# Optimization experiments

Measured on AMD Instinct MI355X. Metric: run time of the kernel, lower is better.

Reference implementation:

```python
import jax, jax.numpy as jnp
import numpy as np

# irreps_in = irreps_out = 32x0e + 16x1o ; irreps_sh = 1x0e + 1x1o
MUL0, MUL1 = 32, 16
N_NODES = 12000
N_EDGES = 120000
INV_SQRT3 = float(1.0 / np.sqrt(3.0))   # w3j(1,1,0), w3j(0,1,1), w3j(1,0,1) coefficient
SQRT2 = float(np.sqrt(2.0))             # e3nn normalize2mom constant for ReLU
# e3nn TP norms: irrep_normalization='component', path_normalization='element'.
# Each output irrep receives paths with num_elements 32 and 16 -> x = 48.
N_0E = float(1.0 / np.sqrt(48.0))       # alpha = dim(0e)/48 = 1/48
N_1O = float(np.sqrt(3.0 / 48.0))       # alpha = dim(1o)/48 = 3/48
# uvw weight blocks (mul2 = 1): (s,y0->s),(s,y0->g),(v,y1->s),(v,y1->g),(s,y1->v),(v,y0->v)
SPLITS = [MUL0 * MUL0, MUL0 * MUL1, MUL1 * MUL0, MUL1 * MUL1, MUL0 * MUL1, MUL1 * MUL1]
OFFS = np.cumsum([0] + SPLITS)
WNUM = int(OFFS[-1])  # 3072


def setup_inputs() -> dict:
    key = jax.random.key(0)
    k1, k2, k3, k4, k5 = jax.random.split(key, 5)
    x = jax.random.normal(k1, (N_NODES, MUL0 + 3 * MUL1), dtype=jnp.float32)
    edge_attr = jax.random.normal(k2, (N_EDGES, 64), dtype=jnp.float32)
    Yij = jax.random.normal(k3, (N_EDGES, 4), dtype=jnp.float32)
    edge_index = jax.random.randint(k4, (2, N_EDGES), 0, N_NODES, dtype=jnp.int64)
    w_emb = jax.random.normal(k5, (2 * MUL0 + 64, WNUM), dtype=jnp.float32)
    return {"x": x, "edge_attr": edge_attr, "Yij": Yij,
            "edge_index": edge_index, "w_emb": w_emb}


def reference(x, edge_attr, Yij, edge_index, w_emb):
    dst, src = edge_index[0], edge_index[1]
    E = edge_attr.shape[0]
    xs = x[:, :MUL0]                                   # [N, 32] scalars (0e)
    xv = x[:, MUL0:].reshape(-1, MUL1, 3)              # [N, 16, 3] vectors (1o)

    # per-edge weight MLP (single e3nn FC layer, weight scaled by 1/sqrt(fan_in))
    emb = jnp.concatenate([xs[dst], xs[src], edge_attr], axis=-1)     # [E, 128]
    w = emb @ (w_emb / np.sqrt(w_emb.shape[0]))                       # [E, 3072]
    Ws = [w[:, OFFS[i]:OFFS[i + 1]] for i in range(6)]
    W1 = Ws[0].reshape(E, MUL0, MUL0)
    W2 = Ws[1].reshape(E, MUL0, MUL1)
    W3 = Ws[2].reshape(E, MUL1, MUL0)
    W4 = Ws[3].reshape(E, MUL1, MUL1)
    W5 = Ws[4].reshape(E, MUL0, MUL1)
    W6 = Ws[5].reshape(E, MUL1, MUL1)

    # gather source features, split sh
    x1s, x1v = xs[src], xv[src]                        # [E,32], [E,16,3]
    y0, y1 = Yij[:, 0], Yij[:, 1:4]                    # [E], [E,3]

    sy0 = x1s * y0[:, None]                            # 0e x 0e paths
    vdot = jnp.einsum('euk,ek->eu', x1v, y1) * INV_SQRT3  # 1o x 1o -> 0e
    out_s = N_0E * (jnp.einsum('euw,eu->ew', W1, sy0) +
                    jnp.einsum('euw,eu->ew', W3, vdot))    # [E, 32]
    out_g = N_0E * (jnp.einsum('euw,eu->ew', W2, sy0) +
                    jnp.einsum('euw,eu->ew', W4, vdot))    # [E, 16]
    out_v = (N_1O * INV_SQRT3) * (
        jnp.einsum('euw,eu,ek->ewk', W5, x1s, y1) +
        jnp.einsum('euw,euk->ewk', W6, x1v * y0[:, None, None]))  # [E, 16, 3]

    msg = jnp.concatenate([out_s, out_g, out_v.reshape(E, MUL1 * 3)], axis=-1)  # [E, 96]

    # scatter mean onto destination nodes
    summed = jax.ops.segment_sum(msg, dst, num_segments=N_NODES)
    cnt = jax.ops.segment_sum(jnp.ones((E,), msg.dtype), dst, num_segments=N_NODES)
    mean = summed / jnp.maximum(cnt, 1.0)[:, None]

    # Gate (e3nn Activation normalizes ReLU by sqrt(2))
    s = SQRT2 * jax.nn.relu(mean[:, :MUL0])
    g = SQRT2 * jax.nn.relu(mean[:, MUL0:MUL0 + MUL1])
    v = mean[:, MUL0 + MUL1:].reshape(-1, MUL1, 3) * g[:, :, None]
    out = jnp.concatenate([s, v.reshape(-1, MUL1 * 3)], axis=-1)     # [N, 80]
    return x + out
```

## Files before the change

### kernel.cpp

```cpp
#include <hip/hip_runtime.h>
#include <hip/hip_bf16.h>

#define E_EDGES 120000
#define NUM_NODES 12000

typedef __attribute__((ext_vector_type(8))) short bfrag;
typedef __attribute__((ext_vector_type(8))) unsigned short ushort8;
typedef __attribute__((ext_vector_type(4))) float f32x4;

#define INV_SQRT3 0.57735026918962576f
#define SQRT2_C   1.41421356237309515f
#define N_0E_C    0.14433756729740643f
#define NV_C      0.14433756729740643f
#define WSCALE    0.08838834764831845f

__device__ __forceinline__ unsigned short f2bf(float f) {
    union { float f; unsigned int u; } v; v.f = f;
    unsigned int r = v.u + 0x7fffu + ((v.u >> 16) & 1u);
    return (unsigned short)(r >> 16);
}

__device__ __forceinline__ ushort8 pack8(f32x4 a, f32x4 b) {
    ushort8 o;
    o[0] = f2bf(a.x); o[1] = f2bf(a.y); o[2] = f2bf(a.z); o[3] = f2bf(a.w);
    o[4] = f2bf(b.x); o[5] = f2bf(b.y); o[6] = f2bf(b.z); o[7] = f2bf(b.w);
    return o;
}

__global__ void k_wt(const float* __restrict__ w_emb, unsigned short* __restrict__ Bt) {
    int o = blockIdx.x * 256 + threadIdx.x;
    if (o >= 3072 * 128) return;
    int t = o >> 11;
    int c = (o >> 3) & 255;
    int j = o & 7;
    int kb = c >> 6;
    int quad = (c >> 4) & 3;
    int col = c & 15;
    int k = kb * 32 + quad * 8 + j;
    int n = t * 16 + col;
    Bt[o] = f2bf(w_emb[k * 3072 + n] * WSCALE);
}

__global__ void k_count(const int* __restrict__ edge_index, int* __restrict__ cnt) {
    int e = blockIdx.x * 256 + threadIdx.x;
    if (e >= E_EDGES) return;
    atomicAdd(cnt + edge_index[e], 1);
}

__global__ void k_scan(const int* __restrict__ cnt, int* __restrict__ offs) {
    __shared__ int psum[256];
    int t = threadIdx.x;
    const int SEG = (NUM_NODES + 255) / 256;
    int lo = t * SEG;
    int hi = lo + SEG; if (hi > NUM_NODES) hi = NUM_NODES;
    int s = 0;
    for (int i = lo; i < hi; ++i) s += cnt[i];
    psum[t] = s;
    __syncthreads();
    if (t == 0) {
        int acc = 0;
        for (int i = 0; i < 256; ++i) { int v = psum[i]; psum[i] = acc; acc += v; }
    }
    __syncthreads();
    int acc = psum[t];
    for (int i = lo; i < hi; ++i) { offs[i] = acc; acc += cnt[i]; }
    if (t == 255) offs[NUM_NODES] = acc;
}

__global__ void k_scatter(const int* __restrict__ edge_index, const int* __restrict__ offs,
                          int* __restrict__ cursor, int* __restrict__ perm_src) {
    int e = blockIdx.x * 256 + threadIdx.x;
    if (e >= E_EDGES) return;
    int d = edge_index[e];
    int p = offs[d] + atomicAdd(cursor + d, 1);
    perm_src[p] = e;
}

__global__ __launch_bounds__(320) void k_prep(
    const float* __restrict__ x, const float* __restrict__ edge_attr,
    const float* __restrict__ Yij, const int* __restrict__ edge_index,
    unsigned short* __restrict__ emb, float* __restrict__ rT) {
    const int wid = threadIdx.x >> 6;
    const int lane = threadIdx.x & 63;
    const long e = (long)blockIdx.x * 64 + lane;
    const int src = edge_index[E_EDGES + e];
    const float* xs = x + (long)src * 80;
    const f32x4 y = *(const f32x4*)(Yij + 4 * e);

    if (wid == 4) {
        const int dst = edge_index[e];
        const float* xd = x + (long)dst * 80;
        const float* ea = edge_attr + (long)e * 64;
        ushort8* embp = (ushort8*)(emb + (long)e * 128);
#pragma unroll
        for (int cb = 0; cb < 4; ++cb)
            embp[cb] = pack8(*(const f32x4*)(xd + cb * 8), *(const f32x4*)(xd + cb * 8 + 4));
#pragma unroll
        for (int cb = 0; cb < 4; ++cb)
            embp[4 + cb] = pack8(*(const f32x4*)(xs + cb * 8), *(const f32x4*)(xs + cb * 8 + 4));
#pragma unroll
        for (int cb = 0; cb < 8; ++cb)
            embp[8 + cb] = pack8(*(const f32x4*)(ea + cb * 8), *(const f32x4*)(ea + cb * 8 + 4));
    } else if (wid == 0) {
        const float y0 = y.x;
#pragma unroll
        for (int i = 0; i < 8; ++i) {
            f32x4 v = *(const f32x4*)(xs + i * 4);
            rT[(long)(4 * i + 0) * E_EDGES + e] = v.x * y0;
            rT[(long)(4 * i + 1) * E_EDGES + e] = v.y * y0;
            rT[(long)(4 * i + 2) * E_EDGES + e] = v.z * y0;
            rT[(long)(4 * i + 3) * E_EDGES + e] = v.w * y0;
        }
    } else if (wid == 1) {
        const float y1a = y.y, y1b = y.z, y1c = y.w;
        float xv[48];
#pragma unroll
        for (int i = 0; i < 12; ++i) {
            f32x4 v = *(const f32x4*)(xs + 32 + i * 4);
            xv[4 * i] = v.x; xv[4 * i + 1] = v.y; xv[4 * i + 2] = v.z; xv[4 * i + 3] = v.w;
        }
#pragma unroll
        for (int u = 0; u < 16; ++u)
            rT[(long)(32 + u) * E_EDGES + e] =
                (xv[3 * u] * y1a + xv[3 * u + 1] * y1b + xv[3 * u + 2] * y1c) * INV_SQRT3;
#pragma unroll
        for (int i = 0; i < 4; ++i) {
            f32x4 v = *(const f32x4*)(xs + i * 4);
            rT[(long)(48 + 4 * i + 0) * E_EDGES + e] = v.x;
            rT[(long)(48 + 4 * i + 1) * E_EDGES + e] = v.y;
            rT[(long)(48 + 4 * i + 2) * E_EDGES + e] = v.z;
            rT[(long)(48 + 4 * i + 3) * E_EDGES + e] = v.w;
        }
    } else if (wid == 2) {
        const float y0 = y.x;
#pragma unroll
        for (int i = 0; i < 4; ++i) {
            f32x4 v = *(const f32x4*)(xs + 16 + i * 4);
            rT[(long)(64 + 4 * i + 0) * E_EDGES + e] = v.x;
            rT[(long)(64 + 4 * i + 1) * E_EDGES + e] = v.y;
            rT[(long)(64 + 4 * i + 2) * E_EDGES + e] = v.z;
            rT[(long)(64 + 4 * i + 3) * E_EDGES + e] = v.w;
        }
#pragma unroll
        for (int i = 0; i < 4; ++i) {
            f32x4 v = *(const f32x4*)(xs + 32 + i * 4);
            rT[(long)(80 + 4 * i + 0) * E_EDGES + e] = v.x * y0;
            rT[(long)(80 + 4 * i + 1) * E_EDGES + e] = v.y * y0;
            rT[(long)(80 + 4 * i + 2) * E_EDGES + e] = v.z * y0;
            rT[(long)(80 + 4 * i + 3) * E_EDGES + e] = v.w * y0;
        }
    } else {
        const float y0 = y.x;
#pragma unroll
        for (int i = 0; i < 8; ++i) {
            f32x4 v = *(const f32x4*)(xs + 48 + i * 4);
            rT[(long)(96 + 4 * i + 0) * E_EDGES + e] = v.x * y0;
            rT[(long)(96 + 4 * i + 1) * E_EDGES + e] = v.y * y0;
            rT[(long)(96 + 4 * i + 2) * E_EDGES + e] = v.z * y0;
            rT[(long)(96 + 4 * i + 3) * E_EDGES + e] = v.w * y0;
        }
    }
}

__global__ __launch_bounds__(256, 4) void k_gemm(
    const unsigned short* __restrict__ emb, const unsigned short* __restrict__ Bt,
    const float* __restrict__ rT, const float* __restrict__ Yij,
    float* __restrict__ msg) {
    const int lane = threadIdx.x & 63;
    const int wave = threadIdx.x >> 6;
    long e0 = (long)blockIdx.x * 128 + (long)wave * 32;
    const bool dup = (e0 + 32 > E_EDGES);
    if (dup) e0 = E_EDGES - 32;
    const int col = lane & 15, quad = lane >> 4;

    __shared__ __align__(16) char lds[2][16384];

    bfrag A[2][4];
#pragma unroll
    for (int s = 0; s < 2; ++s) {
        const unsigned short* ap = emb + (e0 + s * 16 + col) * 128 + quad * 8;
#pragma unroll
        for (int kb = 0; kb < 4; ++kb) A[s][kb] = *(const bfrag*)(ap + kb * 32);
    }

    auto stage = [&](int ci) {
        const char* g = (const char*)Bt + (size_t)ci * 16384 + wave * 4096 + lane * 16;
        char* l = &lds[ci & 1][wave * 4096];
#pragma unroll
        for (int j = 0; j < 4; ++j)
            __builtin_amdgcn_global_load_lds(
                (const __attribute__((address_space(1))) unsigned int*)(g + j * 1024),
                (__attribute__((address_space(3))) unsigned int*)(l + j * 1024), 16, 0, 0);
    };

    f32x4 z = {0.f, 0.f, 0.f, 0.f};
    f32x4 acc_s0[2] = {z, z}, acc_s1[2] = {z, z}, acc_g[2] = {z, z}, acc_t5[2] = {z, z};
    f32x4 acc_v[2][3] = {{z, z, z}, {z, z, z}};

    const float* rbase = rT + e0 + quad * 4;
    auto loadw = [&](int r, f32x4& a, f32x4& b) {
        const float* p = rbase + (long)r * E_EDGES;
        a = *(const f32x4*)(p);
        b = *(const f32x4*)(p + 16);
    };

    auto tile = [&](const char* lt, f32x4& c0, f32x4& c1) {
        bfrag B0 = *(const bfrag*)(lt + lane * 16);
        bfrag B1 = *(const bfrag*)(lt + lane * 16 + 1024);
        bfrag B2 = *(const bfrag*)(lt + lane * 16 + 2048);
        bfrag B3 = *(const bfrag*)(lt + lane * 16 + 3072);
        c0 = z; c1 = z;
        c0 = __builtin_amdgcn_mfma_f32_16x16x32_bf16(A[0][0], B0, c0, 0, 0, 0);
        c1 = __builtin_amdgcn_mfma_f32_16x16x32_bf16(A[1][0], B0, c1, 0, 0, 0);
        c0 = __builtin_amdgcn_mfma_f32_16x16x32_bf16(A[0][1], B1, c0, 0, 0, 0);
        c1 = __builtin_amdgcn_mfma_f32_16x16x32_bf16(A[1][1], B1, c1, 0, 0, 0);
        c0 = __builtin_amdgcn_mfma_f32_16x16x32_bf16(A[0][2], B2, c0, 0, 0, 0);
        c1 = __builtin_amdgcn_mfma_f32_16x16x32_bf16(A[1][2], B2, c1, 0, 0, 0);
        c0 = __builtin_amdgcn_mfma_f32_16x16x32_bf16(A[0][3], B3, c0, 0, 0, 0);
        c1 = __builtin_amdgcn_mfma_f32_16x16x32_bf16(A[1][3], B3, c1, 0, 0, 0);
    };

    stage(0);
    int cidx = 0;
    auto nextbuf = [&]() -> const char* {
        __syncthreads();
        if (cidx + 1 < 48) stage(cidx + 1);
        const char* b = lds[cidx & 1];
        ++cidx;
        return b;
    };

    f32x4 c0, c1;

    {
        f32x4 p0a, p0b, p1a, p1b;
        loadw(0, p0a, p0b); loadw(1, p1a, p1b);
#pragma unroll 1
        for (int j = 0; j < 16; ++j) {
            const char* buf = nextbuf();
            f32x4 w0a = p0a, w0b = p0b, w1a = p1a, w1b = p1b;
            int nr = (j < 15) ? (2 * j + 2) : 0;
            loadw(nr, p0a, p0b); loadw(nr + 1, p1a, p1b);
            tile(buf,         c0, c1); acc_s0[0] += c0 * w0a; acc_s0[1] += c1 * w0b;
            tile(buf + 4096,  c0, c1); acc_s1[0] += c0 * w0a; acc_s1[1] += c1 * w0b;
            tile(buf + 8192,  c0, c1); acc_s0[0] += c0 * w1a; acc_s0[1] += c1 * w1b;
            tile(buf + 12288, c0, c1); acc_s1[0] += c0 * w1a; acc_s1[1] += c1 * w1b;
        }
    }
    {
        f32x4 pa[4], pb[4];
#pragma unroll
        for (int i = 0; i < 4; ++i) loadw(i, pa[i], pb[i]);
#pragma unroll 1
        for (int j = 0; j < 8; ++j) {
            const char* buf = nextbuf();
            f32x4 wa[4], wb[4];
#pragma unroll
            for (int i = 0; i < 4; ++i) { wa[i] = pa[i]; wb[i] = pb[i]; }
            int nr = (j < 7) ? (4 * j + 4) : 0;
#pragma unroll
            for (int i = 0; i < 4; ++i) loadw(nr + i, pa[i], pb[i]);
#pragma unroll
            for (int i = 0; i < 4; ++i) {
                tile(buf + i * 4096, c0, c1);
                acc_g[0] += c0 * wa[i]; acc_g[1] += c1 * wb[i];
            }
        }
    }
    {
        f32x4 p0a, p0b, p1a, p1b;
        loadw(32, p0a, p0b); loadw(33, p1a, p1b);
#pragma unroll 1
        for (int j = 0; j < 8; ++j) {
            const char* buf = nextbuf();
            f32x4 w0a = p0a, w0b = p0b, w1a = p1a, w1b = p1b;
            int nr = (j < 7) ? (32 + 2 * j + 2) : 32;
            loadw(nr, p0a, p0b); loadw(nr + 1, p1a, p1b);
            tile(buf,         c0, c1); acc_s0[0] += c0 * w0a; acc_s0[1] += c1 * w0b;
            tile(buf + 4096,  c0, c1); acc_s1[0] += c0 * w0a; acc_s1[1] += c1 * w0b;
            tile(buf + 8192,  c0, c1); acc_s0[0] += c0 * w1a; acc_s0[1] += c1 * w1b;
            tile(buf + 12288, c0, c1); acc_s1[0] += c0 * w1a; acc_s1[1] += c1 * w1b;
        }
    }
    {
        f32x4 pa[4], pb[4];
#pragma unroll
        for (int i = 0; i < 4; ++i) loadw(32 + i, pa[i], pb[i]);
#pragma unroll 1
        for (int j = 0; j < 4; ++j) {
            const char* buf = nextbuf();
            f32x4 wa[4], wb[4];
#pragma unroll
            for (int i = 0; i < 4; ++i) { wa[i] = pa[i]; wb[i] = pb[i]; }
            int nr = (j < 3) ? (32 + 4 * j + 4) : 32;
#pragma unroll
            for (int i = 0; i < 4; ++i) loadw(nr + i, pa[i], pb[i]);
#pragma unroll
            for (int i = 0; i < 4; ++i) {
                tile(buf + i * 4096, c0, c1);
                acc_g[0] += c0 * wa[i]; acc_g[1] += c1 * wb[i];
            }
        }
    }
    {
        f32x4 pa[4], pb[4];
#pragma unroll
        for (int i = 0; i < 4; ++i) loadw(48 + i, pa[i], pb[i]);
#pragma unroll 1
        for (int j = 0; j < 8; ++j) {
            const char* buf = nextbuf();
            f32x4 wa[4], wb[4];
#pragma unroll
            for (int i = 0; i < 4; ++i) { wa[i] = pa[i]; wb[i] = pb[i]; }
            int nr = (j < 7) ? (48 + 4 * j + 4) : 48;
#pragma unroll
            for (int i = 0; i < 4; ++i) loadw(nr + i, pa[i], pb[i]);
#pragma unroll
            for (int i = 0; i < 4; ++i) {
                tile(buf + i * 4096, c0, c1);
                acc_t5[0] += c0 * wa[i]; acc_t5[1] += c1 * wb[i];
            }
        }
    }
    {
        f32x4 va[3], vb[3];
#pragma unroll
        for (int k = 0; k < 3; ++k) loadw(80 + k, va[k], vb[k]);
#pragma unroll 1
        for (int j = 0; j < 4; ++j) {
            const char* buf = nextbuf();
#pragma unroll
            for (int i = 0; i < 4; ++i) {
                f32x4 wa[3], wb[3];
#pragma unroll
                for (int k = 0; k < 3; ++k) { wa[k] = va[k]; wb[k] = vb[k]; }
                int un = 4 * j + i + 1; if (un > 15) un = 0;
#pragma unroll
                for (int k = 0; k < 3; ++k) loadw(80 + 3 * un + k, va[k], vb[k]);
                tile(buf + i * 4096, c0, c1);
#pragma unroll
                for (int k = 0; k < 3; ++k) {
                    acc_v[0][k] += c0 * wa[k];
                    acc_v[1][k] += c1 * wb[k];
                }
            }
        }
    }

    if (dup) return;
#pragma unroll
    for (int s = 0; s < 2; ++s) {
        long eb = e0 + s * 16 + quad * 4;
#pragma unroll
        for (int r = 0; r < 4; ++r) {
            long e = eb + r;
            float* base = msg + e * 96;
            float y1a = Yij[4 * e + 1], y1b = Yij[4 * e + 2], y1c = Yij[4 * e + 3];
            base[col]            = N_0E_C * acc_s0[s][r];
            base[col + 16]       = N_0E_C * acc_s1[s][r];
            base[32 + col]       = N_0E_C * acc_g[s][r];
            float t5 = acc_t5[s][r];
            base[48 + col * 3 + 0] = NV_C * (t5 * y1a + acc_v[s][0][r]);
            base[48 + col * 3 + 1] = NV_C * (t5 * y1b + acc_v[s][1][r]);
            base[48 + col * 3 + 2] = NV_C * (t5 * y1c + acc_v[s][2][r]);
        }
    }
}

__global__ __launch_bounds__(128) void k_nodesum(
    const float* __restrict__ msg, const int* __restrict__ perm_src,
    const int* __restrict__ offs, const float* __restrict__ x,
    float* __restrict__ out) {
    int n = blockIdx.x;
    int t = threadIdx.x;
    int lo = offs[n], hi = offs[n + 1];
    float s = 0.0f;
    if (t < 96) {
        for (int i = lo; i < hi; ++i) {
            int p = perm_src[i];
            s += msg[(long)p * 96 + t];
        }
    }
    float inv = 1.0f / fmaxf((float)(hi - lo), 1.0f);
    __shared__ float sm[96];
    if (t < 96) sm[t] = s * inv;
    __syncthreads();
    if (t < 80) {
        float val;
        if (t < 32) {
            val = SQRT2_C * fmaxf(sm[t], 0.0f);
        } else {
            int j = t - 32;
            int w = j / 3;
            float g = SQRT2_C * fmaxf(sm[32 + w], 0.0f);
            val = sm[48 + j] * g;
        }
        out[(long)n * 80 + t] = x[(long)n * 80 + t] + val;
    }
}

extern "C" void kernel_launch(void* const* d_in, const int* in_sizes, int n_in,
                              void* d_out, int out_size, void* d_ws, size_t ws_size,
                              hipStream_t stream) {
    const float* x         = (const float*)d_in[0];
    const float* edge_attr = (const float*)d_in[1];
    const float* Yij       = (const float*)d_in[2];
    const int*   edge_index= (const int*)d_in[3];
    const float* w_emb     = (const float*)d_in[4];
    float* out = (float*)d_out;

    char* ws = (char*)d_ws;
    size_t off = 0;
    unsigned short* emb = (unsigned short*)(ws + off); off += (size_t)E_EDGES * 128 * 2;
    unsigned short* Bt  = (unsigned short*)(ws + off); off += (size_t)3072 * 128 * 2;
    off = (off + 255) & ~(size_t)255;
    float* rT      = (float*)(ws + off); off += (size_t)128 * E_EDGES * 4;
    float* msg     = (float*)(ws + off); off += (size_t)E_EDGES * 96 * 4;
    int*   perm_src= (int*)(ws + off);   off += (size_t)E_EDGES * 4;
    int*   offs    = (int*)(ws + off);   off += (size_t)(NUM_NODES + 1) * 4;
    size_t zoff = off;
    int*   cnt     = (int*)(ws + off);   off += (size_t)NUM_NODES * 4;
    int*   cursor  = (int*)(ws + off);   off += (size_t)NUM_NODES * 4;

    hipMemsetAsync(ws + zoff, 0, (size_t)NUM_NODES * 2 * 4, stream);
    k_wt     <<<(3072 * 128 + 255) / 256, 256, 0, stream>>>(w_emb, Bt);
    k_count  <<<(E_EDGES + 255) / 256, 256, 0, stream>>>(edge_index, cnt);
    k_scan   <<<1, 256, 0, stream>>>(cnt, offs);
    k_scatter<<<(E_EDGES + 255) / 256, 256, 0, stream>>>(edge_index, offs, cursor, perm_src);
    k_prep   <<<E_EDGES / 64, 320, 0, stream>>>(x, edge_attr, Yij, edge_index, emb, rT);
    k_gemm   <<<(E_EDGES + 127) / 128, 256, 0, stream>>>(emb, Bt, rT, Yij, msg);
    k_nodesum<<<NUM_NODES, 128, 0, stream>>>(msg, perm_src, offs, x, out);
}
```

Measured before the change: 320.3 us.

## Process edges in destination-sorted order and tile rT per 64-edge block

The prep kernel now reads edges through the destination-sorted permutation. Embeddings, per-edge factors and a copied Yij vector are therefore written in sorted order, so messages come out grouped by destination node. The node reduction can then sum a contiguous run of message rows instead of gathering them through perm_src. The rT buffer also moves from a full-length transposed layout to 64-edge tiles of 128 rows, which keeps the GEMM's per-row loads local. In exchange, edge_attr and Yij reads in prep become random gathers, and a 16-byte-per-edge ys buffer adds write and read traffic.

```diff
diff --git a/kernel.cpp b/kernel.cpp
--- a/kernel.cpp
+++ b/kernel.cpp
@@ -79,19 +79,23 @@
 __global__ __launch_bounds__(320) void k_prep(
     const float* __restrict__ x, const float* __restrict__ edge_attr,
     const float* __restrict__ Yij, const int* __restrict__ edge_index,
-    unsigned short* __restrict__ emb, float* __restrict__ rT) {
+    const int* __restrict__ perm_src,
+    unsigned short* __restrict__ emb, float* __restrict__ rT,
+    f32x4* __restrict__ ys) {
     const int wid = threadIdx.x >> 6;
     const int lane = threadIdx.x & 63;
-    const long e = (long)blockIdx.x * 64 + lane;
-    const int src = edge_index[E_EDGES + e];
+    const long p = (long)blockIdx.x * 64 + lane;
+    const int eid = perm_src[p];
+    const int src = edge_index[E_EDGES + eid];
     const float* xs = x + (long)src * 80;
-    const f32x4 y = *(const f32x4*)(Yij + 4 * e);
+    const f32x4 y = *(const f32x4*)(Yij + 4 * (long)eid);
+    float* tb = rT + (size_t)blockIdx.x * 8192 + lane;
 
     if (wid == 4) {
-        const int dst = edge_index[e];
+        const int dst = edge_index[eid];
         const float* xd = x + (long)dst * 80;
-        const float* ea = edge_attr + (long)e * 64;
-        ushort8* embp = (ushort8*)(emb + (long)e * 128);
+        const float* ea = edge_attr + (long)eid * 64;
+        ushort8* embp = (ushort8*)(emb + (long)p * 128);
 #pragma unroll
         for (int cb = 0; cb < 4; ++cb)
             embp[cb] = pack8(*(const f32x4*)(xd + cb * 8), *(const f32x4*)(xd + cb * 8 + 4));
@@ -106,11 +110,12 @@
 #pragma unroll
         for (int i = 0; i < 8; ++i) {
             f32x4 v = *(const f32x4*)(xs + i * 4);
-            rT[(long)(4 * i + 0) * E_EDGES + e] = v.x * y0;
-            rT[(long)(4 * i + 1) * E_EDGES + e] = v.y * y0;
-            rT[(long)(4 * i + 2) * E_EDGES + e] = v.z * y0;
-            rT[(long)(4 * i + 3) * E_EDGES + e] = v.w * y0;
-        }
+            tb[(4 * i + 0) * 64] = v.x * y0;
+            tb[(4 * i + 1) * 64] = v.y * y0;
+            tb[(4 * i + 2) * 64] = v.z * y0;
+            tb[(4 * i + 3) * 64] = v.w * y0;
+        }
+        ys[p] = y;
     } else if (wid == 1) {
         const float y1a = y.y, y1b = y.z, y1c = y.w;
         float xv[48];
@@ -121,50 +126,50 @@
         }
 #pragma unroll
         for (int u = 0; u < 16; ++u)
-            rT[(long)(32 + u) * E_EDGES + e] =
+            tb[(32 + u) * 64] =
                 (xv[3 * u] * y1a + xv[3 * u + 1] * y1b + xv[3 * u + 2] * y1c) * INV_SQRT3;
 #pragma unroll
         for (int i = 0; i < 4; ++i) {
             f32x4 v = *(const f32x4*)(xs + i * 4);
-            rT[(long)(48 + 4 * i + 0) * E_EDGES + e] = v.x;
-            rT[(long)(48 + 4 * i + 1) * E_EDGES + e] = v.y;
-            rT[(long)(48 + 4 * i + 2) * E_EDGES + e] = v.z;
-            rT[(long)(48 + 4 * i + 3) * E_EDGES + e] = v.w;
+            tb[(48 + 4 * i + 0) * 64] = v.x;
+            tb[(48 + 4 * i + 1) * 64] = v.y;
+            tb[(48 + 4 * i + 2) * 64] = v.z;
+            tb[(48 + 4 * i + 3) * 64] = v.w;
         }
     } else if (wid == 2) {
         const float y0 = y.x;
 #pragma unroll
         for (int i = 0; i < 4; ++i) {
             f32x4 v = *(const f32x4*)(xs + 16 + i * 4);
-            rT[(long)(64 + 4 * i + 0) * E_EDGES + e] = v.x;
-            rT[(long)(64 + 4 * i + 1) * E_EDGES + e] = v.y;
-            rT[(long)(64 + 4 * i + 2) * E_EDGES + e] = v.z;
-            rT[(long)(64 + 4 * i + 3) * E_EDGES + e] = v.w;
+            tb[(64 + 4 * i + 0) * 64] = v.x;
+            tb[(64 + 4 * i + 1) * 64] = v.y;
+            tb[(64 + 4 * i + 2) * 64] = v.z;
+            tb[(64 + 4 * i + 3) * 64] = v.w;
         }
 #pragma unroll
         for (int i = 0; i < 4; ++i) {
             f32x4 v = *(const f32x4*)(xs + 32 + i * 4);
-            rT[(long)(80 + 4 * i + 0) * E_EDGES + e] = v.x * y0;
-            rT[(long)(80 + 4 * i + 1) * E_EDGES + e] = v.y * y0;
-            rT[(long)(80 + 4 * i + 2) * E_EDGES + e] = v.z * y0;
-            rT[(long)(80 + 4 * i + 3) * E_EDGES + e] = v.w * y0;
+            tb[(80 + 4 * i + 0) * 64] = v.x * y0;
+            tb[(80 + 4 * i + 1) * 64] = v.y * y0;
+            tb[(80 + 4 * i + 2) * 64] = v.z * y0;
+            tb[(80 + 4 * i + 3) * 64] = v.w * y0;
         }
     } else {
         const float y0 = y.x;
 #pragma unroll
         for (int i = 0; i < 8; ++i) {
             f32x4 v = *(const f32x4*)(xs + 48 + i * 4);
-            rT[(long)(96 + 4 * i + 0) * E_EDGES + e] = v.x * y0;
-            rT[(long)(96 + 4 * i + 1) * E_EDGES + e] = v.y * y0;
-            rT[(long)(96 + 4 * i + 2) * E_EDGES + e] = v.z * y0;
-            rT[(long)(96 + 4 * i + 3) * E_EDGES + e] = v.w * y0;
+            tb[(96 + 4 * i + 0) * 64] = v.x * y0;
+            tb[(96 + 4 * i + 1) * 64] = v.y * y0;
+            tb[(96 + 4 * i + 2) * 64] = v.z * y0;
+            tb[(96 + 4 * i + 3) * 64] = v.w * y0;
         }
     }
 }
 
 __global__ __launch_bounds__(256, 4) void k_gemm(
     const unsigned short* __restrict__ emb, const unsigned short* __restrict__ Bt,
-    const float* __restrict__ rT, const float* __restrict__ Yij,
+    const float* __restrict__ rT, const f32x4* __restrict__ ys,
     float* __restrict__ msg) {
     const int lane = threadIdx.x & 63;
     const int wave = threadIdx.x >> 6;
@@ -197,9 +202,9 @@
     f32x4 acc_s0[2] = {z, z}, acc_s1[2] = {z, z}, acc_g[2] = {z, z}, acc_t5[2] = {z, z};
     f32x4 acc_v[2][3] = {{z, z, z}, {z, z, z}};
 
-    const float* rbase = rT + e0 + quad * 4;
+    const float* rbase = rT + ((size_t)(e0 >> 6)) * 8192 + (e0 & 32) + quad * 4;
     auto loadw = [&](int r, f32x4& a, f32x4& b) {
-        const float* p = rbase + (long)r * E_EDGES;
+        const float* p = rbase + r * 64;
         a = *(const f32x4*)(p);
         b = *(const f32x4*)(p + 16);
     };
@@ -355,7 +360,8 @@
         for (int r = 0; r < 4; ++r) {
             long e = eb + r;
             float* base = msg + e * 96;
-            float y1a = Yij[4 * e + 1], y1b = Yij[4 * e + 2], y1c = Yij[4 * e + 3];
+            f32x4 y = ys[e];
+            float y1a = y.y, y1b = y.z, y1c = y.w;
             base[col]            = N_0E_C * acc_s0[s][r];
             base[col + 16]       = N_0E_C * acc_s1[s][r];
             base[32 + col]       = N_0E_C * acc_g[s][r];
@@ -368,18 +374,15 @@
 }
 
 __global__ __launch_bounds__(128) void k_nodesum(
-    const float* __restrict__ msg, const int* __restrict__ perm_src,
-    const int* __restrict__ offs, const float* __restrict__ x,
-    float* __restrict__ out) {
+    const float* __restrict__ msg, const int* __restrict__ offs,
+    const float* __restrict__ x, float* __restrict__ out) {
     int n = blockIdx.x;
     int t = threadIdx.x;
     int lo = offs[n], hi = offs[n + 1];
     float s = 0.0f;
     if (t < 96) {
-        for (int i = lo; i < hi; ++i) {
-            int p = perm_src[i];
-            s += msg[(long)p * 96 + t];
-        }
+        const float* mp = msg + (size_t)lo * 96 + t;
+        for (int i = lo; i < hi; ++i, mp += 96) s += *mp;
     }
     float inv = 1.0f / fmaxf((float)(hi - lo), 1.0f);
     __shared__ float sm[96];
@@ -416,6 +419,7 @@
     off = (off + 255) & ~(size_t)255;
     float* rT      = (float*)(ws + off); off += (size_t)128 * E_EDGES * 4;
     float* msg     = (float*)(ws + off); off += (size_t)E_EDGES * 96 * 4;
+    f32x4* ys      = (f32x4*)(ws + off); off += (size_t)E_EDGES * 16;
     int*   perm_src= (int*)(ws + off);   off += (size_t)E_EDGES * 4;
     int*   offs    = (int*)(ws + off);   off += (size_t)(NUM_NODES + 1) * 4;
     size_t zoff = off;
@@ -427,7 +431,8 @@
     k_count  <<<(E_EDGES + 255) / 256, 256, 0, stream>>>(edge_index, cnt);
     k_scan   <<<1, 256, 0, stream>>>(cnt, offs);
     k_scatter<<<(E_EDGES + 255) / 256, 256, 0, stream>>>(edge_index, offs, cursor, perm_src);
-    k_prep   <<<E_EDGES / 64, 320, 0, stream>>>(x, edge_attr, Yij, edge_index, emb, rT);
-    k_gemm   <<<(E_EDGES + 127) / 128, 256, 0, stream>>>(emb, Bt, rT, Yij, msg);
-    k_nodesum<<<NUM_NODES, 128, 0, stream>>>(msg, perm_src, offs, x, out);
-}
+    k_prep   <<<E_EDGES / 64, 320, 0, stream>>>(x, edge_attr, Yij, edge_index, perm_src,
+                                                emb, rT, ys);
+    k_gemm   <<<(E_EDGES + 127) / 128, 256, 0, stream>>>(emb, Bt, rT, ys, msg);
+    k_nodesum<<<NUM_NODES, 128, 0, stream>>>(msg, offs, x, out);
+}
```

Result: faster. 303.7 us (-5.2%).
